# Performance work log

Measured on AMD Instinct MI355X. Metric: run time of the kernel, lower is better.

## Reference

```python
import jax, jax.numpy as jnp
import numpy as np

B, S, D, H = 4, 2048, 1024, 16
DK = D // H
NEG = -1000000000.0


def setup_inputs() -> dict:
    key = jax.random.key(0)
    ks = jax.random.split(key, 12)
    scale = 1.0 / np.sqrt(D)
    inp = {
        "query": jax.random.normal(ks[0], (B, S, D), jnp.float32),
        "key": jax.random.normal(ks[1], (B, S, D), jnp.float32),
        "value": jax.random.normal(ks[2], (B, S, D), jnp.float32),
        "mask": jax.random.randint(ks[3], (B, S, S), 0, 2, jnp.int32),
        "Wq": jax.random.normal(ks[4], (D, D), jnp.float32) * scale,
        "bq": jnp.zeros((D,), jnp.float32),
        "Wk": jax.random.normal(ks[5], (D, D), jnp.float32) * scale,
        "bk": jnp.zeros((D,), jnp.float32),
        "Wv": jax.random.normal(ks[6], (D, D), jnp.float32) * scale,
        "bv": jnp.zeros((D,), jnp.float32),
        "Wo": jax.random.normal(ks[7], (D, D), jnp.float32) * scale,
        "bo": jnp.zeros((D,), jnp.float32),
    }
    return inp


def _split_heads(x):
    # (B, S, D) -> (B, H, S, DK)
    return x.reshape(B, -1, H, DK).transpose(0, 2, 1, 3)


def reference(query, key, value, mask, Wq, bq, Wk, bk, Wv, bv, Wo, bo):
    q = _split_heads(query @ Wq.T + bq)
    k = _split_heads(key @ Wk.T + bk)
    v = _split_heads(value @ Wv.T + bv)
    scores = jnp.einsum('bhqd,bhkd->bhqk', q, k) / jnp.sqrt(jnp.float32(DK))
    scores = jnp.where(mask[:, None, :, :] == 0, NEG, scores)
    p_attn = jax.nn.softmax(scores, axis=-1)
    x = jnp.einsum('bhqk,bhkd->bhqd', p_attn, v)
    x = x.transpose(0, 2, 1, 3).reshape(B, -1, D)
    return x @ Wo.T + bo
```

## Files before the change

kernel.cpp:

```cpp
#include <hip/hip_runtime.h>

#define BDIM 4
#define SDIM 2048
#define DDIM 1024
#define HDIM 16
#define DKDIM 64
#define MDIM (BDIM*SDIM)

typedef __attribute__((ext_vector_type(8))) short bf16x8_t;
typedef __attribute__((ext_vector_type(4))) float f32x4_t;

__device__ __forceinline__ unsigned short f2bf(float f) {
    union { float f; unsigned u; } v; v.f = f;
    unsigned r = v.u + 0x7FFFu + ((v.u >> 16) & 1u);
    return (unsigned short)(r >> 16);
}

__device__ __forceinline__ unsigned pkbf(float a, float b) {
#if defined(__has_builtin) && __has_builtin(__builtin_amdgcn_cvt_pk_bf16_f32)
    auto v = __builtin_amdgcn_cvt_pk_bf16_f32(a, b);
    union { decltype(v) x; unsigned u; } cv; cv.x = v; return cv.u;
#else
    return (unsigned)f2bf(a) | ((unsigned)f2bf(b) << 16);
#endif
}

#if defined(__has_builtin) && __has_builtin(__builtin_amdgcn_exp2f)
#define EXP2F(x) __builtin_amdgcn_exp2f(x)
#else
#define EXP2F(x) __expf((x) * 0.69314718f)
#endif

#define QSCALE 0.18033688011112042f

__device__ __forceinline__ void gl_lds16(const void* g, void* l) {
    __builtin_amdgcn_global_load_lds(
        (const __attribute__((address_space(1))) unsigned int*)g,
        (__attribute__((address_space(3))) unsigned int*)l, 16, 0, 0);
}

__global__ void cvt3(const float* __restrict__ a, const float* __restrict__ b, const float* __restrict__ c,
                     unsigned short* __restrict__ oa, unsigned short* __restrict__ ob, unsigned short* __restrict__ oc,
                     int n4) {
    int i = blockIdx.x * blockDim.x + threadIdx.x;
    const float* s = blockIdx.y == 0 ? a : (blockIdx.y == 1 ? b : c);
    unsigned short* d = blockIdx.y == 0 ? oa : (blockIdx.y == 1 ? ob : oc);
    if (i < n4) {
        float4 v = ((const float4*)s)[i];
        ushort4 o;
        o.x = f2bf(v.x); o.y = f2bf(v.y); o.z = f2bf(v.z); o.w = f2bf(v.w);
        ((ushort4*)d)[i] = o;
    }
}

__global__ void cvt4(const float* __restrict__ a, const float* __restrict__ b,
                     const float* __restrict__ c, const float* __restrict__ e,
                     unsigned short* __restrict__ oa, unsigned short* __restrict__ ob,
                     unsigned short* __restrict__ oc, unsigned short* __restrict__ oe,
                     int n4) {
    int i = blockIdx.x * blockDim.x + threadIdx.x;
    const float* s = blockIdx.y == 0 ? a : (blockIdx.y == 1 ? b : (blockIdx.y == 2 ? c : e));
    unsigned short* d = blockIdx.y == 0 ? oa : (blockIdx.y == 1 ? ob : (blockIdx.y == 2 ? oc : oe));
    if (i < n4) {
        float4 v = ((const float4*)s)[i];
        ushort4 o;
        o.x = f2bf(v.x); o.y = f2bf(v.y); o.z = f2bf(v.z); o.w = f2bf(v.w);
        ((ushort4*)d)[i] = o;
    }
}

__global__ void pack_mask(const int* __restrict__ m, unsigned long long* __restrict__ bits) {
    int g = blockIdx.x * 256 + threadIdx.x;
    unsigned long long bal = __ballot(m[g] != 0);
    if ((threadIdx.x & 63) == 0) bits[g >> 6] = bal;
}

__global__ __launch_bounds__(256) void gemm_qkv(
    const unsigned short* __restrict__ A0, const unsigned short* __restrict__ A1,
    const unsigned short* __restrict__ A2,
    const unsigned short* __restrict__ B0, const unsigned short* __restrict__ B1,
    const unsigned short* __restrict__ B2,
    const float* __restrict__ bi0, const float* __restrict__ bi1, const float* __restrict__ bi2,
    unsigned short* __restrict__ C0, unsigned short* __restrict__ C1,
    unsigned short* __restrict__ C2)
{
    __shared__ unsigned short As[2][128 * 32];
    __shared__ unsigned short Bs[2][128 * 32];
    const int K = DDIM, M = MDIM, N = DDIM;
    const int z = blockIdx.z;
    const unsigned short* A = z == 0 ? A0 : (z == 1 ? A1 : A2);
    const unsigned short* Bw = z == 0 ? B0 : (z == 1 ? B1 : B2);
    const float* bias = z == 0 ? bi0 : (z == 1 ? bi1 : bi2);
    unsigned short* Cb = z == 0 ? C0 : (z == 1 ? C1 : C2);
    const float scale = z == 0 ? QSCALE : 1.0f;

    const int tid = threadIdx.x;
    const int w = tid >> 6, lane = tid & 63;
    const int wr = w >> 1, wc = w & 1;
    const int quad = lane >> 4, l16 = lane & 15;
    const int bn = blockIdx.x, bm = blockIdx.y;

    const int rl = lane >> 2;
    const int cl = (((lane & 3) ^ ((rl >> 1) & 3)) * 8);
    const int sw = (l16 >> 1) & 3;
    const int c0 = w * 2;
    const unsigned short* gA = A + (size_t)(bm * 128 + c0 * 16 + rl) * K + cl;
    const unsigned short* gB = Bw + (size_t)(bn * 128 + c0 * 16 + rl) * K + cl;
    const int ldsoff = c0 * 512 + lane * 8;

    f32x4_t acc[4][4] = {};

    gl_lds16(gA, &As[0][ldsoff]);
    gl_lds16(gA + (size_t)16 * K, &As[0][ldsoff + 16 * 32]);
    gl_lds16(gB, &Bs[0][ldsoff]);
    gl_lds16(gB + (size_t)16 * K, &Bs[0][ldsoff + 16 * 32]);

    int cur = 0;
    for (int k0 = 0; k0 < K; k0 += 32) {
        __syncthreads();
        if (k0 + 32 < K) {
            const unsigned short* nA = gA + k0 + 32;
            const unsigned short* nB = gB + k0 + 32;
            gl_lds16(nA, &As[cur ^ 1][ldsoff]);
            gl_lds16(nA + (size_t)16 * K, &As[cur ^ 1][ldsoff + 16 * 32]);
            gl_lds16(nB, &Bs[cur ^ 1][ldsoff]);
            gl_lds16(nB + (size_t)16 * K, &Bs[cur ^ 1][ldsoff + 16 * 32]);
        }
        bf16x8_t af[4], bfr[4];
#pragma unroll
        for (int mi = 0; mi < 4; ++mi)
            af[mi] = *(const bf16x8_t*)(&As[cur][(wr * 64 + mi * 16 + l16) * 32 + (quad ^ sw) * 8]);
#pragma unroll
        for (int ni = 0; ni < 4; ++ni)
            bfr[ni] = *(const bf16x8_t*)(&Bs[cur][(wc * 64 + ni * 16 + l16) * 32 + (quad ^ sw) * 8]);
#pragma unroll
        for (int mi = 0; mi < 4; ++mi)
#pragma unroll
            for (int ni = 0; ni < 4; ++ni)
                acc[mi][ni] = __builtin_amdgcn_mfma_f32_16x16x32_bf16(af[mi], bfr[ni], acc[mi][ni], 0, 0, 0);
        cur ^= 1;
    }

#pragma unroll
    for (int mi = 0; mi < 4; ++mi) {
#pragma unroll
        for (int ni = 0; ni < 4; ++ni) {
            const int n = bn * 128 + wc * 64 + ni * 16 + l16;
            const int m0 = bm * 128 + wr * 64 + mi * 16 + quad * 4;
            const float bv = bias[n];
            if (z == 2) {
                ushort4 pk;
                pk.x = f2bf(acc[mi][ni][0] + bv);
                pk.y = f2bf(acc[mi][ni][1] + bv);
                pk.z = f2bf(acc[mi][ni][2] + bv);
                pk.w = f2bf(acc[mi][ni][3] + bv);
                *(ushort4*)(Cb + (size_t)n * M + m0) = pk;
            } else {
#pragma unroll
                for (int r = 0; r < 4; ++r)
                    Cb[(size_t)(m0 + r) * N + n] = f2bf((acc[mi][ni][r] + bv) * scale);
            }
        }
    }
}

__global__ __launch_bounds__(256) void gemm_out(
    const unsigned short* __restrict__ A,
    const unsigned short* __restrict__ Bw,
    const float* __restrict__ bias,
    float* __restrict__ Cf)
{
    __shared__ unsigned short As[2][128 * 32];
    __shared__ unsigned short Bs[2][128 * 32];
    const int K = DDIM, N = DDIM;
    const int tid = threadIdx.x;
    const int w = tid >> 6, lane = tid & 63;
    const int wr = w >> 1, wc = w & 1;
    const int quad = lane >> 4, l16 = lane & 15;
    const int bn = blockIdx.x, bm = blockIdx.y;

    const int rl = lane >> 2;
    const int cl = (((lane & 3) ^ ((rl >> 1) & 3)) * 8);
    const int sw = (l16 >> 1) & 3;
    const int c0 = w * 2;
    const unsigned short* gA = A + (size_t)(bm * 128 + c0 * 16 + rl) * K + cl;
    const unsigned short* gB = Bw + (size_t)(bn * 128 + c0 * 16 + rl) * K + cl;
    const int ldsoff = c0 * 512 + lane * 8;

    f32x4_t acc[4][4] = {};

    gl_lds16(gA, &As[0][ldsoff]);
    gl_lds16(gA + (size_t)16 * K, &As[0][ldsoff + 16 * 32]);
    gl_lds16(gB, &Bs[0][ldsoff]);
    gl_lds16(gB + (size_t)16 * K, &Bs[0][ldsoff + 16 * 32]);

    int cur = 0;
    for (int k0 = 0; k0 < K; k0 += 32) {
        __syncthreads();
        if (k0 + 32 < K) {
            const unsigned short* nA = gA + k0 + 32;
            const unsigned short* nB = gB + k0 + 32;
            gl_lds16(nA, &As[cur ^ 1][ldsoff]);
            gl_lds16(nA + (size_t)16 * K, &As[cur ^ 1][ldsoff + 16 * 32]);
            gl_lds16(nB, &Bs[cur ^ 1][ldsoff]);
            gl_lds16(nB + (size_t)16 * K, &Bs[cur ^ 1][ldsoff + 16 * 32]);
        }
        bf16x8_t af[4], bfr[4];
#pragma unroll
        for (int mi = 0; mi < 4; ++mi)
            af[mi] = *(const bf16x8_t*)(&As[cur][(wr * 64 + mi * 16 + l16) * 32 + (quad ^ sw) * 8]);
#pragma unroll
        for (int ni = 0; ni < 4; ++ni)
            bfr[ni] = *(const bf16x8_t*)(&Bs[cur][(wc * 64 + ni * 16 + l16) * 32 + (quad ^ sw) * 8]);
#pragma unroll
        for (int mi = 0; mi < 4; ++mi)
#pragma unroll
            for (int ni = 0; ni < 4; ++ni)
                acc[mi][ni] = __builtin_amdgcn_mfma_f32_16x16x32_bf16(af[mi], bfr[ni], acc[mi][ni], 0, 0, 0);
        cur ^= 1;
    }

#pragma unroll
    for (int mi = 0; mi < 4; ++mi) {
#pragma unroll
        for (int ni = 0; ni < 4; ++ni) {
            const int n = bn * 128 + wc * 64 + ni * 16 + l16;
            const int m0 = bm * 128 + wr * 64 + mi * 16 + quad * 4;
            const float bv = bias[n];
#pragma unroll
            for (int r = 0; r < 4; ++r)
                Cf[(size_t)(m0 + r) * N + n] = acc[mi][ni][r] + bv;
        }
    }
}

__global__ __launch_bounds__(256) void attn_kernel(
    const unsigned short* __restrict__ Qp,
    const unsigned short* __restrict__ Kp,
    const unsigned short* __restrict__ Vt,
    const unsigned long long* __restrict__ mbits,
    unsigned short* __restrict__ Xa)
{
    __shared__ unsigned short SMEM[16384];
    const int tid = threadIdx.x, w = tid >> 6, lane = tid & 63;
    const int quad = lane >> 4, l16 = lane & 15;
    const int bx = blockIdx.x;
    const int h = bx & 15, qt = (bx >> 4) & 15, b = bx >> 8;
    const int q0 = qt * 128;
    const int rl = lane >> 2;
    const int cl = (((lane & 3) ^ ((rl >> 1) & 3)) * 8);
    const int sw = (l16 >> 1) & 3;
    const bool hi16 = (lane & 16) != 0;
    const bool hi32 = (lane & 32) != 0;
    const int idxA = (2 * (quad & 1) + (quad >> 1)) * 16 + l16;
    const int idxC = idxA ^ 16;

#pragma unroll
    for (int i = 0; i < 4; ++i) {
        const int cc = w * 4 + i;
        const int row = b * SDIM + q0 + (cc & 7) * 16 + rl;
        const int col = h * 64 + (cc >> 3) * 32 + cl;
        gl_lds16(Qp + (size_t)row * DDIM + col, SMEM + cc * 512 + lane * 8);
    }
    __syncthreads();
    bf16x8_t aq[2][2];
#pragma unroll
    for (int g = 0; g < 2; ++g)
#pragma unroll
        for (int kk = 0; kk < 2; ++kk)
            aq[g][kk] = *(const bf16x8_t*)(SMEM + (kk * 8 + w * 2 + g) * 512 + l16 * 32 + (quad ^ sw) * 8);
    __syncthreads();

    const unsigned long long* mq0 = mbits + (size_t)(b * SDIM + q0 + w * 32 + l16) * 32;
    const unsigned long long* mq1 = mq0 + (size_t)16 * 32;

#pragma unroll
    for (int i = 0; i < 2; ++i) {
        const int cc = w * 2 + i;
        const int rowk = b * SDIM + (cc & 3) * 16 + rl;
        const int colk = h * 64 + (cc >> 2) * 32 + cl;
        gl_lds16(Kp + (size_t)rowk * DDIM + colk, SMEM + cc * 512 + lane * 8);
        const int rowv = h * 64 + (cc & 3) * 16 + rl;
        const int colv = b * SDIM + (cc >> 2) * 32 + cl;
        gl_lds16(Vt + (size_t)rowv * MDIM + colv, SMEM + 8192 + cc * 512 + lane * 8);
    }
    unsigned long long nm0 = mq0[0], nm1 = mq1[0];

    f32x4_t o[2][4] = {};
    f32x4_t o4[2] = {};
    union { unsigned u[4]; bf16x8_t v; } ones;
    ones.u[0] = ones.u[1] = ones.u[2] = ones.u[3] = 0x3F803F80u;

    int cur = 0;
    for (int kt = 0; kt < SDIM / 64; ++kt) {
        __syncthreads();

        const unsigned long long sh0 = nm0 >> (quad * 4);
        const unsigned long long sh1 = nm1 >> (quad * 4);

        if (kt + 1 < SDIM / 64) {
            const int nb = cur ^ 1;
#pragma unroll
            for (int i = 0; i < 2; ++i) {
                const int cc = w * 2 + i;
                const int rowk = b * SDIM + (kt + 1) * 64 + (cc & 3) * 16 + rl;
                const int colk = h * 64 + (cc >> 2) * 32 + cl;
                gl_lds16(Kp + (size_t)rowk * DDIM + colk, SMEM + nb * 4096 + cc * 512 + lane * 8);
                const int rowv = h * 64 + (cc & 3) * 16 + rl;
                const int colv = b * SDIM + (kt + 1) * 64 + (cc >> 2) * 32 + cl;
                gl_lds16(Vt + (size_t)rowv * MDIM + colv, SMEM + 8192 + nb * 4096 + cc * 512 + lane * 8);
            }
            nm0 = mq0[kt + 1];
            nm1 = mq1[kt + 1];
        }

        const unsigned short* Ksb = SMEM + cur * 4096;
        const unsigned short* Vsb = SMEM + 8192 + cur * 4096;

        f32x4_t sf[2][4] = {};
#pragma unroll
        for (int kk = 0; kk < 2; ++kk) {
#pragma unroll
            for (int ni = 0; ni < 4; ++ni) {
                const bf16x8_t ak = *(const bf16x8_t*)(Ksb + kk * 2048 + (ni * 16 + l16) * 32 + (quad ^ sw) * 8);
                sf[0][ni] = __builtin_amdgcn_mfma_f32_16x16x32_bf16(ak, aq[0][kk], sf[0][ni], 0, 0, 0);
                sf[1][ni] = __builtin_amdgcn_mfma_f32_16x16x32_bf16(ak, aq[1][kk], sf[1][ni], 0, 0, 0);
            }
        }

        unsigned P[2][4][2];
#pragma unroll
        for (int g = 0; g < 2; ++g) {
            const unsigned long long s = g ? sh1 : sh0;
            const unsigned mlo = (unsigned)s, mhi = (unsigned)(s >> 32);
#pragma unroll
            for (int ni = 0; ni < 4; ++ni) {
                const unsigned msel = (ni < 2) ? mlo : mhi;
                const int shf = (ni & 1) * 16;
                float p[4];
#pragma unroll
                for (int r = 0; r < 4; ++r) {
                    const bool on = (msel >> (shf + r)) & 1u;
                    p[r] = EXP2F(on ? sf[g][ni][r] : -1.0e9f);
                }
                P[g][ni][0] = pkbf(p[0], p[1]);
                P[g][ni][1] = pkbf(p[2], p[3]);
            }
        }

#pragma unroll
        for (int kk2 = 0; kk2 < 2; ++kk2) {
            bf16x8_t va[4];
#pragma unroll
            for (int ni = 0; ni < 4; ++ni)
                va[ni] = *(const bf16x8_t*)(Vsb + kk2 * 2048 + (ni * 16 + l16) * 32 + (quad ^ sw) * 8);
#pragma unroll
            for (int g = 0; g < 2; ++g) {
                const unsigned Pa = P[g][kk2 * 2][0], Pb = P[g][kk2 * 2][1];
                const unsigned Pc = P[g][kk2 * 2 + 1][0], Pd = P[g][kk2 * 2 + 1][1];
                const int RA = hi16 ? (int)Pc : (int)Pa;
                const int RB = hi16 ? (int)Pd : (int)Pb;
                const int RC = hi16 ? (int)Pa : (int)Pc;
                const int RD = hi16 ? (int)Pb : (int)Pd;
                const int Av = __shfl(RA, idxA, 64);
                const int Bv = __shfl(RB, idxA, 64);
                const int Cv = __shfl(RC, idxC, 64);
                const int Dv = __shfl(RD, idxC, 64);
                union { unsigned u[4]; bf16x8_t v; } pf;
                pf.u[0] = (unsigned)(hi32 ? Cv : Av);
                pf.u[1] = (unsigned)(hi32 ? Dv : Bv);
                pf.u[2] = (unsigned)(hi32 ? Av : Cv);
                pf.u[3] = (unsigned)(hi32 ? Bv : Dv);
#pragma unroll
                for (int ni = 0; ni < 4; ++ni)
                    o[g][ni] = __builtin_amdgcn_mfma_f32_16x16x32_bf16(va[ni], pf.v, o[g][ni], 0, 0, 0);
                o4[g] = __builtin_amdgcn_mfma_f32_16x16x32_bf16(ones.v, pf.v, o4[g], 0, 0, 0);
            }
        }
        cur ^= 1;
    }

    __syncthreads();
    unsigned short* T = SMEM + w * 1152;
#pragma unroll
    for (int g = 0; g < 2; ++g) {
        const float rcp = 1.0f / o4[g][0];
#pragma unroll
        for (int ni = 0; ni < 4; ++ni) {
            uint2 pk;
            pk.x = pkbf(o[g][ni][0] * rcp, o[g][ni][1] * rcp);
            pk.y = pkbf(o[g][ni][2] * rcp, o[g][ni][3] * rcp);
            *(uint2*)&T[l16 * 72 + ni * 16 + quad * 4] = pk;
        }
        const int qrow = q0 + w * 32 + g * 16 + (lane >> 2);
        const int dkc = (lane & 3) * 16;
        __syncthreads();
        const bf16x8_t r0 = *(const bf16x8_t*)&T[(lane >> 2) * 72 + dkc];
        const bf16x8_t r1 = *(const bf16x8_t*)&T[(lane >> 2) * 72 + dkc + 8];
        unsigned short* dst = Xa + (size_t)(b * SDIM + qrow) * DDIM + h * 64 + dkc;
        *(bf16x8_t*)dst = r0;
        *(bf16x8_t*)(dst + 8) = r1;
        __syncthreads();
    }
}

extern "C" void kernel_launch(void* const* d_in, const int* in_sizes, int n_in,
                              void* d_out, int out_size, void* d_ws, size_t ws_size,
                              hipStream_t stream)
{
    const float* query = (const float*)d_in[0];
    const float* key   = (const float*)d_in[1];
    const float* value = (const float*)d_in[2];
    const int*   mask  = (const int*)d_in[3];
    const float* Wq = (const float*)d_in[4];  const float* bq = (const float*)d_in[5];
    const float* Wk = (const float*)d_in[6];  const float* bk = (const float*)d_in[7];
    const float* Wv = (const float*)d_in[8];  const float* bv = (const float*)d_in[9];
    const float* Wo = (const float*)d_in[10]; const float* bo = (const float*)d_in[11];

    const size_t MD = (size_t)MDIM * DDIM;
    const size_t DD = (size_t)DDIM * DDIM;

    unsigned short* qb  = (unsigned short*)d_ws;
    unsigned short* kb  = qb + MD;
    unsigned short* vb  = kb + MD;
    unsigned short* wqb = vb + MD;
    unsigned short* wkb = wqb + DD;
    unsigned short* wvb = wkb + DD;
    unsigned short* wob = wvb + DD;
    unsigned short* Qp  = wob + DD;
    unsigned short* Kp  = Qp + MD;
    unsigned short* Vt  = Kp + MD;
    unsigned short* Xa  = Vt + MD;
    unsigned long long* mbits = (unsigned long long*)qb;

    {
        const int n4m = (int)(MD / 4), n4d = (int)(DD / 4);
        dim3 g3((n4m + 255) / 256, 3), g4((n4d + 255) / 256, 4);
        cvt3<<<g3, 256, 0, stream>>>(query, key, value, qb, kb, vb, n4m);
        cvt4<<<g4, 256, 0, stream>>>(Wq, Wk, Wv, Wo, wqb, wkb, wvb, wob, n4d);
    }

    dim3 gq(DDIM / 128, MDIM / 128, 3);
    gemm_qkv<<<gq, 256, 0, stream>>>(qb, kb, vb, wqb, wkb, wvb, bq, bk, bv, Qp, Kp, Vt);

    pack_mask<<<(BDIM * SDIM * SDIM) / 256, 256, 0, stream>>>(mask, mbits);

    attn_kernel<<<BDIM * HDIM * (SDIM / 128), 256, 0, stream>>>(Qp, Kp, Vt, mbits, Xa);

    dim3 gg(DDIM / 128, MDIM / 128);
    gemm_out<<<gg, 256, 0, stream>>>(Xa, wob, bo, (float*)d_out);
}
```

Baseline: 463.3 us.

## Rewrite attention inner loop with 32x32x16 MFMA and permlane32 swaps

Reworks the attention kernel to use 32x32x16 bf16 MFMAs instead of 16x16x32. Q fragments now load directly from global memory into registers, and the P-fragment transpose uses v_permlane32_swap in place of four cross-lane shuffles. Masking becomes a bitwise AND on the exponentiated value, and the epilogue is simplified with fewer barriers. Separately, bf16 conversions switch to inline v_cvt_pk_bf16_f32 asm and the attention kernel gets a launch-bounds occupancy hint. The larger accumulators raise register pressure, and the inline asm relies on gfx950-specific instructions.

```diff
diff --git a/kernel.cpp b/kernel.cpp
--- a/kernel.cpp
+++ b/kernel.cpp
@@ -9,6 +9,7 @@
 
 typedef __attribute__((ext_vector_type(8))) short bf16x8_t;
 typedef __attribute__((ext_vector_type(4))) float f32x4_t;
+typedef __attribute__((ext_vector_type(16))) float f32x16_t;
 
 __device__ __forceinline__ unsigned short f2bf(float f) {
     union { float f; unsigned u; } v; v.f = f;
@@ -17,12 +18,13 @@
 }
 
 __device__ __forceinline__ unsigned pkbf(float a, float b) {
-#if defined(__has_builtin) && __has_builtin(__builtin_amdgcn_cvt_pk_bf16_f32)
-    auto v = __builtin_amdgcn_cvt_pk_bf16_f32(a, b);
-    union { decltype(v) x; unsigned u; } cv; cv.x = v; return cv.u;
-#else
-    return (unsigned)f2bf(a) | ((unsigned)f2bf(b) << 16);
-#endif
+    unsigned r;
+    asm("v_cvt_pk_bf16_f32 %0, %1, %2" : "=v"(r) : "v"(a), "v"(b));
+    return r;
+}
+
+__device__ __forceinline__ void plswap(unsigned &a, unsigned &b) {
+    asm("v_permlane32_swap_b32 %0, %1" : "+v"(a), "+v"(b));
 }
 
 #if defined(__has_builtin) && __has_builtin(__builtin_amdgcn_exp2f)
@@ -47,9 +49,10 @@
     unsigned short* d = blockIdx.y == 0 ? oa : (blockIdx.y == 1 ? ob : oc);
     if (i < n4) {
         float4 v = ((const float4*)s)[i];
-        ushort4 o;
-        o.x = f2bf(v.x); o.y = f2bf(v.y); o.z = f2bf(v.z); o.w = f2bf(v.w);
-        ((ushort4*)d)[i] = o;
+        uint2 o;
+        o.x = pkbf(v.x, v.y);
+        o.y = pkbf(v.z, v.w);
+        ((uint2*)d)[i] = o;
     }
 }
 
@@ -63,9 +66,10 @@
     unsigned short* d = blockIdx.y == 0 ? oa : (blockIdx.y == 1 ? ob : (blockIdx.y == 2 ? oc : oe));
     if (i < n4) {
         float4 v = ((const float4*)s)[i];
-        ushort4 o;
-        o.x = f2bf(v.x); o.y = f2bf(v.y); o.z = f2bf(v.z); o.w = f2bf(v.w);
-        ((ushort4*)d)[i] = o;
+        uint2 o;
+        o.x = pkbf(v.x, v.y);
+        o.y = pkbf(v.z, v.w);
+        ((uint2*)d)[i] = o;
     }
 }
 
@@ -149,16 +153,17 @@
             const int m0 = bm * 128 + wr * 64 + mi * 16 + quad * 4;
             const float bv = bias[n];
             if (z == 2) {
-                ushort4 pk;
-                pk.x = f2bf(acc[mi][ni][0] + bv);
-                pk.y = f2bf(acc[mi][ni][1] + bv);
-                pk.z = f2bf(acc[mi][ni][2] + bv);
-                pk.w = f2bf(acc[mi][ni][3] + bv);
-                *(ushort4*)(Cb + (size_t)n * M + m0) = pk;
+                uint2 pk2;
+                pk2.x = pkbf(acc[mi][ni][0] + bv, acc[mi][ni][1] + bv);
+                pk2.y = pkbf(acc[mi][ni][2] + bv, acc[mi][ni][3] + bv);
+                *(uint2*)(Cb + (size_t)n * M + m0) = pk2;
             } else {
-#pragma unroll
-                for (int r = 0; r < 4; ++r)
-                    Cb[(size_t)(m0 + r) * N + n] = f2bf((acc[mi][ni][r] + bv) * scale);
+                unsigned pa = pkbf((acc[mi][ni][0] + bv) * scale, (acc[mi][ni][1] + bv) * scale);
+                unsigned pb = pkbf((acc[mi][ni][2] + bv) * scale, (acc[mi][ni][3] + bv) * scale);
+                Cb[(size_t)(m0 + 0) * N + n] = (unsigned short)pa;
+                Cb[(size_t)(m0 + 1) * N + n] = (unsigned short)(pa >> 16);
+                Cb[(size_t)(m0 + 2) * N + n] = (unsigned short)pb;
+                Cb[(size_t)(m0 + 3) * N + n] = (unsigned short)(pb >> 16);
             }
         }
     }
@@ -234,7 +239,7 @@
     }
 }
 
-__global__ __launch_bounds__(256) void attn_kernel(
+__global__ __launch_bounds__(256, 4) void attn_kernel(
     const unsigned short* __restrict__ Qp,
     const unsigned short* __restrict__ Kp,
     const unsigned short* __restrict__ Vt,
@@ -243,165 +248,118 @@
 {
     __shared__ unsigned short SMEM[16384];
     const int tid = threadIdx.x, w = tid >> 6, lane = tid & 63;
-    const int quad = lane >> 4, l16 = lane & 15;
+    const int l32 = lane & 31, hi = lane >> 5;
     const int bx = blockIdx.x;
     const int h = bx & 15, qt = (bx >> 4) & 15, b = bx >> 8;
     const int q0 = qt * 128;
     const int rl = lane >> 2;
     const int cl = (((lane & 3) ^ ((rl >> 1) & 3)) * 8);
-    const int sw = (l16 >> 1) & 3;
-    const bool hi16 = (lane & 16) != 0;
-    const bool hi32 = (lane & 32) != 0;
-    const int idxA = (2 * (quad & 1) + (quad >> 1)) * 16 + l16;
-    const int idxC = idxA ^ 16;
-
-#pragma unroll
-    for (int i = 0; i < 4; ++i) {
-        const int cc = w * 4 + i;
-        const int row = b * SDIM + q0 + (cc & 7) * 16 + rl;
-        const int col = h * 64 + (cc >> 3) * 32 + cl;
-        gl_lds16(Qp + (size_t)row * DDIM + col, SMEM + cc * 512 + lane * 8);
-    }
-    __syncthreads();
-    bf16x8_t aq[2][2];
-#pragma unroll
-    for (int g = 0; g < 2; ++g)
-#pragma unroll
-        for (int kk = 0; kk < 2; ++kk)
-            aq[g][kk] = *(const bf16x8_t*)(SMEM + (kk * 8 + w * 2 + g) * 512 + l16 * 32 + (quad ^ sw) * 8);
-    __syncthreads();
-
-    const unsigned long long* mq0 = mbits + (size_t)(b * SDIM + q0 + w * 32 + l16) * 32;
-    const unsigned long long* mq1 = mq0 + (size_t)16 * 32;
-
-#pragma unroll
-    for (int i = 0; i < 2; ++i) {
-        const int cc = w * 2 + i;
-        const int rowk = b * SDIM + (cc & 3) * 16 + rl;
-        const int colk = h * 64 + (cc >> 2) * 32 + cl;
-        gl_lds16(Kp + (size_t)rowk * DDIM + colk, SMEM + cc * 512 + lane * 8);
-        const int rowv = h * 64 + (cc & 3) * 16 + rl;
-        const int colv = b * SDIM + (cc >> 2) * 32 + cl;
-        gl_lds16(Vt + (size_t)rowv * MDIM + colv, SMEM + 8192 + cc * 512 + lane * 8);
-    }
-    unsigned long long nm0 = mq0[0], nm1 = mq1[0];
-
-    f32x4_t o[2][4] = {};
-    f32x4_t o4[2] = {};
+    const int swl = (l32 >> 1) & 3;
+    const int lbase = (l32 >> 4) * 512 + (l32 & 15) * 32 + ((hi ^ swl) * 8);
+    const int myq = b * SDIM + q0 + w * 32 + l32;
+
+    bf16x8_t qf[4];
+    {
+        const unsigned short* gq = Qp + (size_t)myq * DDIM + h * 64 + hi * 8;
+#pragma unroll
+        for (int c = 0; c < 4; ++c)
+            qf[c] = *(const bf16x8_t*)(gq + c * 16);
+    }
+
+    const unsigned long long* mq = mbits + (size_t)myq * 32;
+
+    const int cc0 = w * 2, cc1 = w * 2 + 1;
+    const unsigned short* gK0 = Kp + (size_t)(b * SDIM + (cc0 & 3) * 16 + rl) * DDIM + h * 64 + (cc0 >> 2) * 32 + cl;
+    const unsigned short* gK1 = Kp + (size_t)(b * SDIM + (cc1 & 3) * 16 + rl) * DDIM + h * 64 + (cc1 >> 2) * 32 + cl;
+    const unsigned short* gV0 = Vt + (size_t)(h * 64 + (cc0 & 3) * 16 + rl) * MDIM + b * SDIM + (cc0 >> 2) * 32 + cl;
+    const unsigned short* gV1 = Vt + (size_t)(h * 64 + (cc1 & 3) * 16 + rl) * MDIM + b * SDIM + (cc1 >> 2) * 32 + cl;
+    unsigned short* dK0 = SMEM + cc0 * 512 + lane * 8;
+    unsigned short* dK1 = SMEM + cc1 * 512 + lane * 8;
+    unsigned short* dV0 = SMEM + 8192 + cc0 * 512 + lane * 8;
+    unsigned short* dV1 = SMEM + 8192 + cc1 * 512 + lane * 8;
+
+    gl_lds16(gK0, dK0);
+    gl_lds16(gK1, dK1);
+    gl_lds16(gV0, dV0);
+    gl_lds16(gV1, dV1);
+    unsigned long long nm = mq[0];
+
+    f32x16_t o0 = {}, o1 = {}, o4 = {};
     union { unsigned u[4]; bf16x8_t v; } ones;
     ones.u[0] = ones.u[1] = ones.u[2] = ones.u[3] = 0x3F803F80u;
 
     int cur = 0;
     for (int kt = 0; kt < SDIM / 64; ++kt) {
         __syncthreads();
-
-        const unsigned long long sh0 = nm0 >> (quad * 4);
-        const unsigned long long sh1 = nm1 >> (quad * 4);
+        const unsigned long long mysh = nm >> (4 * hi);
+        const unsigned mw0 = (unsigned)mysh;
+        const unsigned mw1 = (unsigned)(mysh >> 32);
 
         if (kt + 1 < SDIM / 64) {
-            const int nb = cur ^ 1;
-#pragma unroll
-            for (int i = 0; i < 2; ++i) {
-                const int cc = w * 2 + i;
-                const int rowk = b * SDIM + (kt + 1) * 64 + (cc & 3) * 16 + rl;
-                const int colk = h * 64 + (cc >> 2) * 32 + cl;
-                gl_lds16(Kp + (size_t)rowk * DDIM + colk, SMEM + nb * 4096 + cc * 512 + lane * 8);
-                const int rowv = h * 64 + (cc & 3) * 16 + rl;
-                const int colv = b * SDIM + (kt + 1) * 64 + (cc >> 2) * 32 + cl;
-                gl_lds16(Vt + (size_t)rowv * MDIM + colv, SMEM + 8192 + nb * 4096 + cc * 512 + lane * 8);
-            }
-            nm0 = mq0[kt + 1];
-            nm1 = mq1[kt + 1];
-        }
-
+            const int nb = (cur ^ 1) * 4096;
+            const size_t ko = (size_t)(kt + 1) * 64 * DDIM;
+            const size_t vo = (size_t)(kt + 1) * 64;
+            gl_lds16(gK0 + ko, dK0 + nb);
+            gl_lds16(gK1 + ko, dK1 + nb);
+            gl_lds16(gV0 + vo, dV0 + nb);
+            gl_lds16(gV1 + vo, dV1 + nb);
+            nm = mq[kt + 1];
+        }
         const unsigned short* Ksb = SMEM + cur * 4096;
         const unsigned short* Vsb = SMEM + 8192 + cur * 4096;
 
-        f32x4_t sf[2][4] = {};
-#pragma unroll
-        for (int kk = 0; kk < 2; ++kk) {
-#pragma unroll
-            for (int ni = 0; ni < 4; ++ni) {
-                const bf16x8_t ak = *(const bf16x8_t*)(Ksb + kk * 2048 + (ni * 16 + l16) * 32 + (quad ^ sw) * 8);
-                sf[0][ni] = __builtin_amdgcn_mfma_f32_16x16x32_bf16(ak, aq[0][kk], sf[0][ni], 0, 0, 0);
-                sf[1][ni] = __builtin_amdgcn_mfma_f32_16x16x32_bf16(ak, aq[1][kk], sf[1][ni], 0, 0, 0);
+#pragma unroll
+        for (int t = 0; t < 2; ++t) {
+            f32x16_t s = {};
+#pragma unroll
+            for (int c = 0; c < 4; ++c) {
+                const bf16x8_t ak = *(const bf16x8_t*)(Ksb + (c >> 1) * 2048 + t * 1024 + (lbase ^ ((c & 1) * 16)));
+                s = __builtin_amdgcn_mfma_f32_32x32x16_bf16(ak, qf[c], s, 0, 0, 0);
             }
-        }
-
-        unsigned P[2][4][2];
-#pragma unroll
-        for (int g = 0; g < 2; ++g) {
-            const unsigned long long s = g ? sh1 : sh0;
-            const unsigned mlo = (unsigned)s, mhi = (unsigned)(s >> 32);
-#pragma unroll
-            for (int ni = 0; ni < 4; ++ni) {
-                const unsigned msel = (ni < 2) ? mlo : mhi;
-                const int shf = (ni & 1) * 16;
-                float p[4];
-#pragma unroll
-                for (int r = 0; r < 4; ++r) {
-                    const bool on = (msel >> (shf + r)) & 1u;
-                    p[r] = EXP2F(on ? sf[g][ni][r] : -1.0e9f);
-                }
-                P[g][ni][0] = pkbf(p[0], p[1]);
-                P[g][ni][1] = pkbf(p[2], p[3]);
+            const unsigned wm = t ? mw1 : mw0;
+            float p[16];
+#pragma unroll
+            for (int r = 0; r < 16; ++r) {
+                const int pos = (r & 3) + 8 * (r >> 2);
+                const float pe = EXP2F(s[r]);
+                const int mm = (int)(wm << (31 - pos)) >> 31;
+                p[r] = __uint_as_float(__float_as_uint(pe) & (unsigned)mm);
             }
-        }
-
-#pragma unroll
-        for (int kk2 = 0; kk2 < 2; ++kk2) {
-            bf16x8_t va[4];
-#pragma unroll
-            for (int ni = 0; ni < 4; ++ni)
-                va[ni] = *(const bf16x8_t*)(Vsb + kk2 * 2048 + (ni * 16 + l16) * 32 + (quad ^ sw) * 8);
-#pragma unroll
-            for (int g = 0; g < 2; ++g) {
-                const unsigned Pa = P[g][kk2 * 2][0], Pb = P[g][kk2 * 2][1];
-                const unsigned Pc = P[g][kk2 * 2 + 1][0], Pd = P[g][kk2 * 2 + 1][1];
-                const int RA = hi16 ? (int)Pc : (int)Pa;
-                const int RB = hi16 ? (int)Pd : (int)Pb;
-                const int RC = hi16 ? (int)Pa : (int)Pc;
-                const int RD = hi16 ? (int)Pb : (int)Pd;
-                const int Av = __shfl(RA, idxA, 64);
-                const int Bv = __shfl(RB, idxA, 64);
-                const int Cv = __shfl(RC, idxC, 64);
-                const int Dv = __shfl(RD, idxC, 64);
+#pragma unroll
+            for (int c2 = 0; c2 < 2; ++c2) {
+                unsigned d0 = pkbf(p[c2 * 8 + 0], p[c2 * 8 + 1]);
+                unsigned d1 = pkbf(p[c2 * 8 + 2], p[c2 * 8 + 3]);
+                unsigned d2 = pkbf(p[c2 * 8 + 4], p[c2 * 8 + 5]);
+                unsigned d3 = pkbf(p[c2 * 8 + 6], p[c2 * 8 + 7]);
+                plswap(d0, d2);
+                plswap(d1, d3);
                 union { unsigned u[4]; bf16x8_t v; } pf;
-                pf.u[0] = (unsigned)(hi32 ? Cv : Av);
-                pf.u[1] = (unsigned)(hi32 ? Dv : Bv);
-                pf.u[2] = (unsigned)(hi32 ? Av : Cv);
-                pf.u[3] = (unsigned)(hi32 ? Bv : Dv);
-#pragma unroll
-                for (int ni = 0; ni < 4; ++ni)
-                    o[g][ni] = __builtin_amdgcn_mfma_f32_16x16x32_bf16(va[ni], pf.v, o[g][ni], 0, 0, 0);
-                o4[g] = __builtin_amdgcn_mfma_f32_16x16x32_bf16(ones.v, pf.v, o4[g], 0, 0, 0);
+                pf.u[0] = d0; pf.u[1] = d1; pf.u[2] = d2; pf.u[3] = d3;
+                const bf16x8_t va0 = *(const bf16x8_t*)(Vsb + t * 2048 + (lbase ^ (c2 * 16)));
+                const bf16x8_t va1 = *(const bf16x8_t*)(Vsb + t * 2048 + 1024 + (lbase ^ (c2 * 16)));
+                o0 = __builtin_amdgcn_mfma_f32_32x32x16_bf16(va0, pf.v, o0, 0, 0, 0);
+                o1 = __builtin_amdgcn_mfma_f32_32x32x16_bf16(va1, pf.v, o1, 0, 0, 0);
+                o4 = __builtin_amdgcn_mfma_f32_32x32x16_bf16(ones.v, pf.v, o4, 0, 0, 0);
             }
         }
         cur ^= 1;
     }
 
     __syncthreads();
-    unsigned short* T = SMEM + w * 1152;
-#pragma unroll
-    for (int g = 0; g < 2; ++g) {
-        const float rcp = 1.0f / o4[g][0];
-#pragma unroll
-        for (int ni = 0; ni < 4; ++ni) {
-            uint2 pk;
-            pk.x = pkbf(o[g][ni][0] * rcp, o[g][ni][1] * rcp);
-            pk.y = pkbf(o[g][ni][2] * rcp, o[g][ni][3] * rcp);
-            *(uint2*)&T[l16 * 72 + ni * 16 + quad * 4] = pk;
-        }
-        const int qrow = q0 + w * 32 + g * 16 + (lane >> 2);
-        const int dkc = (lane & 3) * 16;
-        __syncthreads();
-        const bf16x8_t r0 = *(const bf16x8_t*)&T[(lane >> 2) * 72 + dkc];
-        const bf16x8_t r1 = *(const bf16x8_t*)&T[(lane >> 2) * 72 + dkc + 8];
-        unsigned short* dst = Xa + (size_t)(b * SDIM + qrow) * DDIM + h * 64 + dkc;
-        *(bf16x8_t*)dst = r0;
-        *(bf16x8_t*)(dst + 8) = r1;
-        __syncthreads();
-    }
+    unsigned short* T = SMEM + w * 2304;
+    const float rcp = 1.0f / o4[0];
+#pragma unroll
+    for (int pi = 0; pi < 8; ++pi) {
+        const int dk = (pi & 1) * 2 + 8 * (pi >> 1) + 4 * hi;
+        *(unsigned*)&T[l32 * 72 + dk]      = pkbf(o0[2 * pi] * rcp, o0[2 * pi + 1] * rcp);
+        *(unsigned*)&T[l32 * 72 + 32 + dk] = pkbf(o1[2 * pi] * rcp, o1[2 * pi + 1] * rcp);
+    }
+    const int rrow = lane >> 1;
+    const unsigned short* Trow = SMEM + w * 2304 + rrow * 72 + (lane & 1) * 32;
+    unsigned short* dst = Xa + (size_t)(b * SDIM + q0 + w * 32 + rrow) * DDIM + h * 64 + (lane & 1) * 32;
+#pragma unroll
+    for (int i = 0; i < 4; ++i)
+        *(bf16x8_t*)(dst + i * 8) = *(const bf16x8_t*)(Trow + i * 8);
 }
 
 extern "C" void kernel_launch(void* const* d_in, const int* in_sizes, int n_in,
```

Result: faster. 419.5 us (-9.4%).
